# Optimization experiments

Measured on AMD Instinct MI355X. Metric: run time of the kernel, lower is better.

The kernel has to match this reference:

```python
import jax, jax.numpy as jnp
import numpy as np


def setup_inputs() -> dict:
    key = jax.random.key(0)
    k1, k2 = jax.random.split(key)
    B, C, H, W = 32, 2, 512, 512
    inp = jax.random.normal(k1, (B, C, H, W), dtype=jnp.float32)
    tgt = jax.random.normal(k2, (B, C, H, W), dtype=jnp.float32)
    return {"input": inp, "target": tgt}


def reference(input, target):
    B, C, H, W = input.shape
    # normalized coordinate grids: (j+1)/W along x, (p+1)/H along y
    xg = jnp.arange(1, W + 1, dtype=input.dtype) / W  # (W,)
    yg = jnp.arange(1, H + 1, dtype=input.dtype) / H  # (H,)
    # softmax over flattened heatmap per (b, c)
    p = jax.nn.softmax(input.reshape(B, C, H * W), axis=-1).reshape(B, C, H, W)
    # soft-argmax coords in normalized units, then scaled to pixels (*W, *H)
    pred_x = jnp.einsum('bchw,w->bc', p, xg) * W
    pred_y = jnp.einsum('bchw,h->bc', p, yg) * H
    # ground truth: hard argmax of target heatmap -> pixel coords
    idx = jnp.argmax(target.reshape(B, C, H * W), axis=-1)
    true_x = (idx % W + 1).astype(input.dtype)   # ((idx%W+1)/W)*W
    true_y = (idx // W + 1).astype(input.dtype)  # ((idx//W+1)/H)*H
    ed = jnp.sqrt((true_x - pred_x) ** 2 + (true_y - pred_y) ** 2)  # (B, C)
    s_i = jnp.sum(ed[:, 0])   # channel 0 -> inferior
    s_s = jnp.sum(ed[:, 1:])  # remaining channels -> superior
    denom = jnp.asarray(B, input.dtype)
    return (s_i / denom, s_s / denom, (s_i + s_s) / denom)
```

## Files before the change

kernel.cpp:

```cpp
#include <hip/hip_runtime.h>
#include <math.h>

constexpr int Wd      = 512;
constexpr int Hd      = 512;
constexpr int HW      = Wd * Hd;
constexpr int NBC     = 64;
constexpr int SPLITS  = 32;
constexpr int CHUNK   = HW / SPLITS;
constexpr int NPART   = NBC * SPLITS;
constexpr int THREADS = 256;


__global__ __launch_bounds__(THREADS) void dsnt_pass1(
    const float* __restrict__ inp, const float* __restrict__ tgt,
    float* __restrict__ ws) {
  const int bid   = blockIdx.x;
  const int bc    = bid >> 5;
  const int split = bid & (SPLITS - 1);
  const int t     = threadIdx.x;

  const float4* ip4 = (const float4*)(inp + (size_t)bc * HW + (size_t)split * CHUNK);
  const float4* tp4 = (const float4*)(tgt + (size_t)bc * HW + (size_t)split * CHUNK);
  const int rbase = split * CHUNK;

  float l0 = 0.f, l1 = 0.f, l2 = 0.f, l3 = 0.f;
  float sx0 = 0.f, sx1 = 0.f, sx2 = 0.f, sx3 = 0.f;
  float sy0 = 0.f, sy1 = 0.f, sy2 = 0.f, sy3 = 0.f;
  float tv = -INFINITY;
  int   ti = 0;

#pragma unroll
  for (int batch = 0; batch < 2; ++batch) {
    float4 a[4], b[4];
#pragma unroll
    for (int i = 0; i < 4; ++i) {
      const int q = t + (batch * 4 + i) * THREADS;
      a[i] = ip4[q];
      b[i] = tp4[q];
    }
#pragma unroll
    for (int i = 0; i < 4; ++i) {
      const int q = t + (batch * 4 + i) * THREADS;
      const int r = rbase + q * 4;
      const float yc = (float)((r >> 9) + 1);
      const float x0 = (float)((r & 511) + 1);

      const float e0 = __expf(a[i].x);
      const float e1 = __expf(a[i].y);
      const float e2 = __expf(a[i].z);
      const float e3 = __expf(a[i].w);
      l0 += e0; l1 += e1; l2 += e2; l3 += e3;
      sx0 = fmaf(e0, x0,       sx0);
      sx1 = fmaf(e1, x0 + 1.f, sx1);
      sx2 = fmaf(e2, x0 + 2.f, sx2);
      sx3 = fmaf(e3, x0 + 3.f, sx3);
      sy0 = fmaf(e0, yc, sy0);
      sy1 = fmaf(e1, yc, sy1);
      sy2 = fmaf(e2, yc, sy2);
      sy3 = fmaf(e3, yc, sy3);

      if (b[i].x > tv) { tv = b[i].x; ti = r; }
      if (b[i].y > tv) { tv = b[i].y; ti = r + 1; }
      if (b[i].z > tv) { tv = b[i].z; ti = r + 2; }
      if (b[i].w > tv) { tv = b[i].w; ti = r + 3; }
    }
  }

  float l  = (l0 + l1) + (l2 + l3);
  float sx = (sx0 + sx1) + (sx2 + sx3);
  float sy = (sy0 + sy1) + (sy2 + sy3);

#pragma unroll
  for (int off = 32; off; off >>= 1) {
    l  += __shfl_xor(l, off);
    sx += __shfl_xor(sx, off);
    sy += __shfl_xor(sy, off);
    const float tv2 = __shfl_xor(tv, off);
    const int   ti2 = __shfl_xor(ti, off);
    if (tv2 > tv || (tv2 == tv && ti2 < ti)) { tv = tv2; ti = ti2; }
  }

  __shared__ float sml[4], smx[4], smy[4], smv[4];
  __shared__ int   smi[4];
  const int wave = t >> 6;
  if ((t & 63) == 0) {
    sml[wave] = l; smx[wave] = sx; smy[wave] = sy;
    smv[wave] = tv; smi[wave] = ti;
  }
  __syncthreads();
  if (t == 0) {
#pragma unroll
    for (int wv = 1; wv < 4; ++wv) {
      l += sml[wv]; sx += smx[wv]; sy += smy[wv];
      const float tv2 = smv[wv];
      const int   ti2 = smi[wv];
      if (tv2 > tv || (tv2 == tv && ti2 < ti)) { tv = tv2; ti = ti2; }
    }
    float* Pl = ws;
    float* Px = ws + NPART;
    float* Py = ws + 2 * NPART;
    float* Pv = ws + 3 * NPART;
    int*   Pi = (int*)(ws + 4 * NPART);
    Pl[bid] = l; Px[bid] = sx; Py[bid] = sy;
    Pv[bid] = tv; Pi[bid] = ti;
  }
}

__global__ __launch_bounds__(256) void dsnt_pass2(const float* __restrict__ ws,
                                                  float* __restrict__ out) {
  const int t    = threadIdx.x;
  const int bc   = t >> 2;
  const int part = t & 3;
  const float* Pl = ws;
  const float* Px = ws + NPART;
  const float* Py = ws + 2 * NPART;
  const float* Pv = ws + 3 * NPART;
  const int*   Pi = (const int*)(ws + 4 * NPART);

  float l = 0.f, sx = 0.f, sy = 0.f;
  float tv = -INFINITY;
  int   ti = 0x7fffffff;
#pragma unroll
  for (int j = 0; j < 8; ++j) {
    const int p = bc * SPLITS + part * 8 + j;
    l  += Pl[p];
    sx += Px[p];
    sy += Py[p];
    const float v  = Pv[p];
    const int   ix = Pi[p];
    if (v > tv || (v == tv && ix < ti)) { tv = v; ti = ix; }
  }
#pragma unroll
  for (int off = 1; off <= 2; off <<= 1) {
    l  += __shfl_xor(l, off);
    sx += __shfl_xor(sx, off);
    sy += __shfl_xor(sy, off);
    const float tv2 = __shfl_xor(tv, off);
    const int   ti2 = __shfl_xor(ti, off);
    if (tv2 > tv || (tv2 == tv && ti2 < ti)) { tv = tv2; ti = ti2; }
  }

  __shared__ float edArr[NBC];
  if (part == 0) {
    const float predx = sx / l;
    const float predy = sy / l;
    const float truex = (float)((ti & 511) + 1);
    const float truey = (float)((ti >> 9) + 1);
    const float dx = truex - predx, dy = truey - predy;
    edArr[bc] = sqrtf(dx * dx + dy * dy);
  }
  __syncthreads();
  if (t < NBC) {
    const float ed = edArr[t];
    float ei = (t & 1) ? 0.f : ed;
    float es = (t & 1) ? ed : 0.f;
#pragma unroll
    for (int off = 32; off; off >>= 1) {
      ei += __shfl_xor(ei, off);
      es += __shfl_xor(es, off);
    }
    if (t == 0) {
      out[0] = ei * (1.f / 32.f);
      out[1] = es * (1.f / 32.f);
      out[2] = (ei + es) * (1.f / 32.f);
    }
  }
}

extern "C" void kernel_launch(void* const* d_in, const int* in_sizes, int n_in,
                              void* d_out, int out_size, void* d_ws, size_t ws_size,
                              hipStream_t stream) {
  const float* inp = (const float*)d_in[0];
  const float* tgt = (const float*)d_in[1];
  float* out = (float*)d_out;
  float* ws  = (float*)d_ws;

  dsnt_pass1<<<NPART, THREADS, 0, stream>>>(inp, tgt, ws);
  dsnt_pass2<<<1, 256, 0, stream>>>(ws, out);
}
```

Before: 149.1 us.

## Split pass1 into separate softmax and argmax block roles

Doubles the pass1 grid so half the blocks compute the exp-weighted sums over the input and the other half compute the argmax over the target. Each block now loads all of its chunk at once, eight float4 loads per thread from a single tensor. The aim is more blocks and more memory parallelism, with a shorter dependency chain per block. The cost is more register pressure from the eight-element load array, plus extra block scheduling and reduction overhead.

```diff
diff --git a/kernel.cpp b/kernel.cpp
--- a/kernel.cpp
+++ b/kernel.cpp
@@ -9,100 +9,104 @@
 constexpr int CHUNK   = HW / SPLITS;
 constexpr int NPART   = NBC * SPLITS;
 constexpr int THREADS = 256;
+constexpr int F4_PER_T = CHUNK / 4 / THREADS;
 
 
 __global__ __launch_bounds__(THREADS) void dsnt_pass1(
     const float* __restrict__ inp, const float* __restrict__ tgt,
     float* __restrict__ ws) {
   const int bid   = blockIdx.x;
-  const int bc    = bid >> 5;
-  const int split = bid & (SPLITS - 1);
+  const int role  = bid >> 11;
+  const int sub   = bid & 2047;
+  const int bc    = sub >> 5;
+  const int split = sub & (SPLITS - 1);
   const int t     = threadIdx.x;
-
-  const float4* ip4 = (const float4*)(inp + (size_t)bc * HW + (size_t)split * CHUNK);
-  const float4* tp4 = (const float4*)(tgt + (size_t)bc * HW + (size_t)split * CHUNK);
   const int rbase = split * CHUNK;
 
-  float l0 = 0.f, l1 = 0.f, l2 = 0.f, l3 = 0.f;
-  float sx0 = 0.f, sx1 = 0.f, sx2 = 0.f, sx3 = 0.f;
-  float sy0 = 0.f, sy1 = 0.f, sy2 = 0.f, sy3 = 0.f;
-  float tv = -INFINITY;
-  int   ti = 0;
+  __shared__ float sm0[4], sm1[4], sm2[4];
+  __shared__ int   smi[4];
+  const int wave = t >> 6;
 
+  float* Pl = ws;
+  float* Px = ws + NPART;
+  float* Py = ws + 2 * NPART;
+  float* Pv = ws + 3 * NPART;
+  int*   Pi = (int*)(ws + 4 * NPART);
+
+  if (role == 0) {
+    const float4* ip4 = (const float4*)(inp + (size_t)bc * HW + (size_t)rbase);
+    float4 a[F4_PER_T];
 #pragma unroll
-  for (int batch = 0; batch < 2; ++batch) {
-    float4 a[4], b[4];
+    for (int i = 0; i < F4_PER_T; ++i) a[i] = ip4[t + i * THREADS];
+
+    float lA = 0.f, lB = 0.f, sxA = 0.f, sxB = 0.f, syA = 0.f, syB = 0.f;
 #pragma unroll
-    for (int i = 0; i < 4; ++i) {
-      const int q = t + (batch * 4 + i) * THREADS;
-      a[i] = ip4[q];
-      b[i] = tp4[q];
-    }
-#pragma unroll
-    for (int i = 0; i < 4; ++i) {
-      const int q = t + (batch * 4 + i) * THREADS;
-      const int r = rbase + q * 4;
+    for (int i = 0; i < F4_PER_T; ++i) {
+      const int r = rbase + (t + i * THREADS) * 4;
       const float yc = (float)((r >> 9) + 1);
       const float x0 = (float)((r & 511) + 1);
-
       const float e0 = __expf(a[i].x);
       const float e1 = __expf(a[i].y);
       const float e2 = __expf(a[i].z);
       const float e3 = __expf(a[i].w);
-      l0 += e0; l1 += e1; l2 += e2; l3 += e3;
-      sx0 = fmaf(e0, x0,       sx0);
-      sx1 = fmaf(e1, x0 + 1.f, sx1);
-      sx2 = fmaf(e2, x0 + 2.f, sx2);
-      sx3 = fmaf(e3, x0 + 3.f, sx3);
-      sy0 = fmaf(e0, yc, sy0);
-      sy1 = fmaf(e1, yc, sy1);
-      sy2 = fmaf(e2, yc, sy2);
-      sy3 = fmaf(e3, yc, sy3);
-
-      if (b[i].x > tv) { tv = b[i].x; ti = r; }
-      if (b[i].y > tv) { tv = b[i].y; ti = r + 1; }
-      if (b[i].z > tv) { tv = b[i].z; ti = r + 2; }
-      if (b[i].w > tv) { tv = b[i].w; ti = r + 3; }
+      lA += e0 + e2;
+      lB += e1 + e3;
+      sxA = fmaf(e0, x0,       sxA);  sxA = fmaf(e2, x0 + 2.f, sxA);
+      sxB = fmaf(e1, x0 + 1.f, sxB);  sxB = fmaf(e3, x0 + 3.f, sxB);
+      syA = fmaf(e0 + e2, yc, syA);
+      syB = fmaf(e1 + e3, yc, syB);
     }
-  }
-
-  float l  = (l0 + l1) + (l2 + l3);
-  float sx = (sx0 + sx1) + (sx2 + sx3);
-  float sy = (sy0 + sy1) + (sy2 + sy3);
+    float l = lA + lB, sx = sxA + sxB, sy = syA + syB;
 
 #pragma unroll
-  for (int off = 32; off; off >>= 1) {
-    l  += __shfl_xor(l, off);
-    sx += __shfl_xor(sx, off);
-    sy += __shfl_xor(sy, off);
-    const float tv2 = __shfl_xor(tv, off);
-    const int   ti2 = __shfl_xor(ti, off);
-    if (tv2 > tv || (tv2 == tv && ti2 < ti)) { tv = tv2; ti = ti2; }
-  }
+    for (int off = 32; off; off >>= 1) {
+      l  += __shfl_xor(l, off);
+      sx += __shfl_xor(sx, off);
+      sy += __shfl_xor(sy, off);
+    }
+    if ((t & 63) == 0) { sm0[wave] = l; sm1[wave] = sx; sm2[wave] = sy; }
+    __syncthreads();
+    if (t == 0) {
+#pragma unroll
+      for (int wv = 1; wv < 4; ++wv) { l += sm0[wv]; sx += sm1[wv]; sy += sm2[wv]; }
+      Pl[sub] = l; Px[sub] = sx; Py[sub] = sy;
+    }
+  } else {
+    const float4* tp4 = (const float4*)(tgt + (size_t)bc * HW + (size_t)rbase);
+    float4 b[F4_PER_T];
+#pragma unroll
+    for (int i = 0; i < F4_PER_T; ++i) b[i] = tp4[t + i * THREADS];
 
-  __shared__ float sml[4], smx[4], smy[4], smv[4];
-  __shared__ int   smi[4];
-  const int wave = t >> 6;
-  if ((t & 63) == 0) {
-    sml[wave] = l; smx[wave] = sx; smy[wave] = sy;
-    smv[wave] = tv; smi[wave] = ti;
-  }
-  __syncthreads();
-  if (t == 0) {
+    float tvA = -INFINITY, tvB = -INFINITY;
+    int   tiA = 0, tiB = 0;
 #pragma unroll
-    for (int wv = 1; wv < 4; ++wv) {
-      l += sml[wv]; sx += smx[wv]; sy += smy[wv];
-      const float tv2 = smv[wv];
-      const int   ti2 = smi[wv];
+    for (int i = 0; i < F4_PER_T; ++i) {
+      const int r = rbase + (t + i * THREADS) * 4;
+      if (b[i].x > tvA) { tvA = b[i].x; tiA = r; }
+      if (b[i].z > tvA) { tvA = b[i].z; tiA = r + 2; }
+      if (b[i].y > tvB) { tvB = b[i].y; tiB = r + 1; }
+      if (b[i].w > tvB) { tvB = b[i].w; tiB = r + 3; }
+    }
+    float tv = tvA; int ti = tiA;
+    if (tvB > tv || (tvB == tv && tiB < ti)) { tv = tvB; ti = tiB; }
+
+#pragma unroll
+    for (int off = 32; off; off >>= 1) {
+      const float tv2 = __shfl_xor(tv, off);
+      const int   ti2 = __shfl_xor(ti, off);
       if (tv2 > tv || (tv2 == tv && ti2 < ti)) { tv = tv2; ti = ti2; }
     }
-    float* Pl = ws;
-    float* Px = ws + NPART;
-    float* Py = ws + 2 * NPART;
-    float* Pv = ws + 3 * NPART;
-    int*   Pi = (int*)(ws + 4 * NPART);
-    Pl[bid] = l; Px[bid] = sx; Py[bid] = sy;
-    Pv[bid] = tv; Pi[bid] = ti;
+    if ((t & 63) == 0) { sm0[wave] = tv; smi[wave] = ti; }
+    __syncthreads();
+    if (t == 0) {
+#pragma unroll
+      for (int wv = 1; wv < 4; ++wv) {
+        const float tv2 = sm0[wv];
+        const int   ti2 = smi[wv];
+        if (tv2 > tv || (tv2 == tv && ti2 < ti)) { tv = tv2; ti = ti2; }
+      }
+      Pv[sub] = tv; Pi[sub] = ti;
+    }
   }
 }
 
@@ -175,6 +179,6 @@
   float* out = (float*)d_out;
   float* ws  = (float*)d_ws;
 
-  dsnt_pass1<<<NPART, THREADS, 0, stream>>>(inp, tgt, ws);
+  dsnt_pass1<<<2 * NPART, THREADS, 0, stream>>>(inp, tgt, ws);
   dsnt_pass2<<<1, 256, 0, stream>>>(ws, out);
 }
```

Result: no change. 148.0 us, median of 2 (-0.8%).
